# Performance work log

Measured on AMD Instinct MI355X. Metric: run time of the kernel, lower is better.

The kernel has to match this reference:

```python
import jax, jax.numpy as jnp
import numpy as np

NUM_NEURONS = 8192
INPUT_SIZE = 512
OUTPUT_SIZE = 512
TAU = 10.0
G = 1.5


def setup_inputs() -> dict:
    key = jax.random.key(0)
    k1, k2, k3, k4, k5 = jax.random.split(key, 5)
    inputs = jax.random.normal(k1, (INPUT_SIZE,), dtype=jnp.float32)
    potentials = jax.random.normal(k2, (1, NUM_NEURONS), dtype=jnp.float32)
    # parameters, matching the torch init scales
    W_in = jax.random.normal(k3, (INPUT_SIZE, NUM_NEURONS), dtype=jnp.float32) * 0.1
    synapses = jax.random.normal(k4, (NUM_NEURONS, NUM_NEURONS), dtype=jnp.float32) / np.sqrt(NUM_NEURONS).astype(np.float32)
    W_out = jax.random.normal(k5, (NUM_NEURONS, OUTPUT_SIZE), dtype=jnp.float32) / np.float32(NUM_NEURONS)
    return {"inputs": inputs, "potentials": potentials, "W_in": W_in,
            "synapses": synapses, "W_out": W_out}


def reference(inputs, potentials, W_in, synapses, W_out):
    # input_map: bias-free linear, then unsqueeze to [1, N]
    drive = (inputs @ W_in)[None, :]                      # [1, N]
    # Neurons: continuous-time leaky integrator (FORCE-style)
    rates = jnp.tanh(potentials)                          # [1, N]
    pot_new = potentials + (-potentials + G * (rates @ synapses) + drive) / TAU
    gen_net = jnp.tanh(pot_new)                           # [1, N]
    # read_out: bias-free linear
    output = gen_net @ W_out                              # [1, output_size]
    return (output, pot_new)
```

## Files before the change

kernel.cpp:

```cpp
#include <hip/hip_runtime.h>
#include <math.h>

#define N_NEU   8192
#define IN_SZ   512
#define OUT_SZ  512
#define N4      (N_NEU / 4)
#define OUT4    (OUT_SZ / 4)
#define KPB     128
#define WPB     8
#define SYN_TILES (N_NEU / KPB)
#define K2_KPB  32
#define OTILES  (N_NEU / K2_KPB)
constexpr float TAU_INV = 0.1f;
constexpr float G_GAIN  = 1.5f;

__global__ __launch_bounds__(256)
void zero_kernel(float* __restrict__ out) {
    out[blockIdx.x * 256 + threadIdx.x] = 0.0f;
}

__global__ __launch_bounds__(256)
void accum_kernel(const float* __restrict__ pot,
                  const float* __restrict__ inputs,
                  const float* __restrict__ synapses,
                  const float* __restrict__ W_in,
                  float* __restrict__ out) {
    __shared__ float xs[KPB + WPB];
    const int bx = blockIdx.x, by = blockIdx.y;
    const int tid = threadIdx.x;
    const int k0 = by * KPB;
    const int w0 = by * WPB;
    if (tid < KPB)                xs[tid] = G_GAIN * tanhf(pot[k0 + tid]);
    else if (tid < KPB + WPB)     xs[tid] = inputs[w0 + (tid - KPB)];
    __syncthreads();

    const int col4 = bx * 256 + tid;
    const float4* Sp = (const float4*)synapses + (size_t)k0 * N4 + col4;
    const float4* Wp = (const float4*)W_in     + (size_t)w0 * N4 + col4;

    float4 acc = make_float4(0.f, 0.f, 0.f, 0.f);
#pragma unroll 8
    for (int i = 0; i < KPB; ++i) {
        float  s = xs[i];
        float4 m = Sp[(size_t)i * N4];
        acc.x = fmaf(s, m.x, acc.x);
        acc.y = fmaf(s, m.y, acc.y);
        acc.z = fmaf(s, m.z, acc.z);
        acc.w = fmaf(s, m.w, acc.w);
    }
#pragma unroll
    for (int i = 0; i < WPB; ++i) {
        float  s = xs[KPB + i];
        float4 m = Wp[(size_t)i * N4];
        acc.x = fmaf(s, m.x, acc.x);
        acc.y = fmaf(s, m.y, acc.y);
        acc.z = fmaf(s, m.z, acc.z);
        acc.w = fmaf(s, m.w, acc.w);
    }
    float* op = out + OUT_SZ + (size_t)col4 * 4;
    atomicAdd(op + 0, acc.x);
    atomicAdd(op + 1, acc.y);
    atomicAdd(op + 2, acc.z);
    atomicAdd(op + 3, acc.w);
}

__global__ __launch_bounds__(128)
void finish_kernel(const float* __restrict__ pot,
                   const float* __restrict__ W_out,
                   float* __restrict__ out) {
    __shared__ float xs[K2_KPB];
    const int b = blockIdx.x;
    const int t = threadIdx.x;
    const int k0 = b * K2_KPB;

    if (t < K2_KPB) {
        float s  = out[OUT_SZ + k0 + t];
        float p  = pot[k0 + t];
        float pn = p + (s - p) * TAU_INV;
        out[OUT_SZ + k0 + t] = pn;
        xs[t] = tanhf(pn);
    }
    __syncthreads();

    const float4* Wp = (const float4*)W_out + (size_t)k0 * OUT4 + t;
    float4 acc = make_float4(0.f, 0.f, 0.f, 0.f);
#pragma unroll 8
    for (int i = 0; i < K2_KPB; ++i) {
        float  sx = xs[i];
        float4 m  = Wp[(size_t)i * OUT4];
        acc.x = fmaf(sx, m.x, acc.x);
        acc.y = fmaf(sx, m.y, acc.y);
        acc.z = fmaf(sx, m.z, acc.z);
        acc.w = fmaf(sx, m.w, acc.w);
    }
    float* op = out + (size_t)t * 4;
    atomicAdd(op + 0, acc.x);
    atomicAdd(op + 1, acc.y);
    atomicAdd(op + 2, acc.z);
    atomicAdd(op + 3, acc.w);
}

extern "C" void kernel_launch(void* const* d_in, const int* in_sizes, int n_in,
                              void* d_out, int out_size, void* d_ws, size_t ws_size,
                              hipStream_t stream) {
    const float* inputs   = (const float*)d_in[0];
    const float* pot      = (const float*)d_in[1];
    const float* W_in     = (const float*)d_in[2];
    const float* synapses = (const float*)d_in[3];
    const float* W_out    = (const float*)d_in[4];

    float* out = (float*)d_out;
    (void)d_ws; (void)ws_size;

    zero_kernel<<<dim3((OUT_SZ + N_NEU) / 256), dim3(256), 0, stream>>>(out);

    accum_kernel<<<dim3(8, SYN_TILES), dim3(256), 0, stream>>>(
        pot, inputs, synapses, W_in, out);

    finish_kernel<<<dim3(OTILES), dim3(128), 0, stream>>>(pot, W_out, out);
}
```

Baseline: 406.9 us.

## Replace atomic split-K reduction with workspace partials reduced in finish kernel

The accumulate kernel now writes each K-tile's partial sums to a workspace buffer instead of doing float atomics into the output. The finish kernel reduces the 64 partials per neuron before the leaky-integrator update. Zeroing of the output head moves into the first accumulate block, which drops the separate zero kernel launch. Finish blocks now cover 64 rows with 256 threads and combine two halves in shared memory, halving the readout atomics. In exchange it adds about 2 MB of partial-sum write and read traffic and relies on the workspace being large enough.

```diff
diff --git a/kernel.cpp b/kernel.cpp
--- a/kernel.cpp
+++ b/kernel.cpp
@@ -9,21 +9,17 @@
 #define KPB     128
 #define WPB     8
 #define SYN_TILES (N_NEU / KPB)
-#define K2_KPB  32
-#define OTILES  (N_NEU / K2_KPB)
+#define K2_ROWS 64
+#define K2_BLKS (N_NEU / K2_ROWS)
 constexpr float TAU_INV = 0.1f;
 constexpr float G_GAIN  = 1.5f;
-
-__global__ __launch_bounds__(256)
-void zero_kernel(float* __restrict__ out) {
-    out[blockIdx.x * 256 + threadIdx.x] = 0.0f;
-}
 
 __global__ __launch_bounds__(256)
 void accum_kernel(const float* __restrict__ pot,
                   const float* __restrict__ inputs,
                   const float* __restrict__ synapses,
                   const float* __restrict__ W_in,
+                  float4* __restrict__ P4,
                   float* __restrict__ out) {
     __shared__ float xs[KPB + WPB];
     const int bx = blockIdx.x, by = blockIdx.y;
@@ -32,6 +28,8 @@
     const int w0 = by * WPB;
     if (tid < KPB)                xs[tid] = G_GAIN * tanhf(pot[k0 + tid]);
     else if (tid < KPB + WPB)     xs[tid] = inputs[w0 + (tid - KPB)];
+    if (bx == 0 && by == 0 && tid < 128)
+        ((float4*)out)[tid] = make_float4(0.f, 0.f, 0.f, 0.f);
     __syncthreads();
 
     const int col4 = bx * 256 + tid;
@@ -57,47 +55,63 @@
         acc.z = fmaf(s, m.z, acc.z);
         acc.w = fmaf(s, m.w, acc.w);
     }
-    float* op = out + OUT_SZ + (size_t)col4 * 4;
-    atomicAdd(op + 0, acc.x);
-    atomicAdd(op + 1, acc.y);
-    atomicAdd(op + 2, acc.z);
-    atomicAdd(op + 3, acc.w);
+    P4[(size_t)by * N4 + col4] = acc;
 }
 
-__global__ __launch_bounds__(128)
+__global__ __launch_bounds__(256)
 void finish_kernel(const float* __restrict__ pot,
+                   const float* __restrict__ P,
                    const float* __restrict__ W_out,
                    float* __restrict__ out) {
-    __shared__ float xs[K2_KPB];
+    __shared__ float  red[256];
+    __shared__ float  xs[K2_ROWS];
+    __shared__ float4 hi[128];
     const int b = blockIdx.x;
     const int t = threadIdx.x;
-    const int k0 = b * K2_KPB;
+    const int k0 = b * K2_ROWS;
+    const int r = t & 63;
+    const int q = t >> 6;
 
-    if (t < K2_KPB) {
-        float s  = out[OUT_SZ + k0 + t];
-        float p  = pot[k0 + t];
-        float pn = p + (s - p) * TAU_INV;
+    float s = 0.f;
+#pragma unroll
+    for (int p = 0; p < 16; ++p)
+        s += P[(size_t)(q * 16 + p) * N_NEU + k0 + r];
+    red[t] = s;
+    __syncthreads();
+
+    if (t < K2_ROWS) {
+        float drive = red[t] + red[64 + t] + red[128 + t] + red[192 + t];
+        float pv = pot[k0 + t];
+        float pn = pv + (drive - pv) * TAU_INV;
         out[OUT_SZ + k0 + t] = pn;
         xs[t] = tanhf(pn);
     }
     __syncthreads();
 
-    const float4* Wp = (const float4*)W_out + (size_t)k0 * OUT4 + t;
+    const int c4 = t & 127;
+    const int h  = t >> 7;
+    const float4* Wp = (const float4*)W_out + (size_t)(k0 + h * 32) * OUT4 + c4;
     float4 acc = make_float4(0.f, 0.f, 0.f, 0.f);
 #pragma unroll 8
-    for (int i = 0; i < K2_KPB; ++i) {
-        float  sx = xs[i];
+    for (int i = 0; i < 32; ++i) {
+        float  sx = xs[h * 32 + i];
         float4 m  = Wp[(size_t)i * OUT4];
         acc.x = fmaf(sx, m.x, acc.x);
         acc.y = fmaf(sx, m.y, acc.y);
         acc.z = fmaf(sx, m.z, acc.z);
         acc.w = fmaf(sx, m.w, acc.w);
     }
-    float* op = out + (size_t)t * 4;
-    atomicAdd(op + 0, acc.x);
-    atomicAdd(op + 1, acc.y);
-    atomicAdd(op + 2, acc.z);
-    atomicAdd(op + 3, acc.w);
+    if (h == 1) hi[c4] = acc;
+    __syncthreads();
+    if (h == 0) {
+        float4 o = hi[c4];
+        acc.x += o.x; acc.y += o.y; acc.z += o.z; acc.w += o.w;
+        float* op = out + (size_t)c4 * 4;
+        atomicAdd(op + 0, acc.x);
+        atomicAdd(op + 1, acc.y);
+        atomicAdd(op + 2, acc.z);
+        atomicAdd(op + 3, acc.w);
+    }
 }
 
 extern "C" void kernel_launch(void* const* d_in, const int* in_sizes, int n_in,
@@ -110,12 +124,11 @@
     const float* W_out    = (const float*)d_in[4];
 
     float* out = (float*)d_out;
-    (void)d_ws; (void)ws_size;
-
-    zero_kernel<<<dim3((OUT_SZ + N_NEU) / 256), dim3(256), 0, stream>>>(out);
+    float* P   = (float*)d_ws;
 
     accum_kernel<<<dim3(8, SYN_TILES), dim3(256), 0, stream>>>(
-        pot, inputs, synapses, W_in, out);
+        pot, inputs, synapses, W_in, (float4*)P, out);
 
-    finish_kernel<<<dim3(OTILES), dim3(128), 0, stream>>>(pot, W_out, out);
+    finish_kernel<<<dim3(K2_BLKS), dim3(256), 0, stream>>>(
+        pot, P, W_out, out);
 }
```

New measurement: 392.0 us. -3.7%, faster.
